# Kernel optimization log

Hardware: AMD Instinct MI355X
Metric: run time of the kernel (lower is better)

Reference implementation:

```python
import jax, jax.numpy as jnp
import numpy as np
from jax.scipy.special import gammaln

S, N, T = 8, 32, 262144
EPS = 1e-16  # emission clamp, as in torch .clamp(min=1e-16)


def setup_inputs() -> dict:
    key = jax.random.key(0)
    k1, k2, k3, k4 = jax.random.split(key, 4)
    spikes = jax.random.randint(k1, (T, N), 0, 2).astype(jnp.int32)  # binary counts
    convolved_spikes = 0.5 * jax.random.normal(k2, (T, N), dtype=jnp.float32)
    weight = 0.1 * jax.random.normal(k3, (S, N, N), dtype=jnp.float32)
    bias = 0.1 * jax.random.normal(k4, (N,), dtype=jnp.float32)
    eye = jnp.eye(S, dtype=jnp.float32)
    transition_matrix = eye * 0.98 + (0.02 / (S - 1)) * (1.0 - eye)
    return {"spikes": spikes, "convolved_spikes": convolved_spikes,
            "weight": weight, "bias": bias, "transition_matrix": transition_matrix}


def reference(spikes, convolved_spikes, weight, bias, transition_matrix):
    n_states = weight.shape[0]
    init_p = jnp.ones(n_states, dtype=convolved_spikes.dtype) / n_states
    A = transition_matrix  # (S, S)

    # firing_rates: sigmoid(bias + conv @ W[s].T) -> (S, T, N)
    rates = jax.nn.sigmoid(bias[None, None, :] +
                           jnp.einsum('tn,smn->stm', convolved_spikes, weight))
    x = spikes.astype(rates.dtype)
    # Poisson log-likelihood summed over neurons, then (S,T) -> (T,S)
    log_emission = (x[None] * jnp.log(rates) - rates - gammaln(x + 1.0)[None]).sum(-1).T

    emission = jnp.clip(jnp.exp(log_emission), EPS)  # (T, S)

    # forward pass (scaling)
    a0 = init_p * emission[0]
    c0 = a0.sum()
    a0 = a0 / c0

    def fstep(a_prev, em_t):
        a = em_t * (A.T @ a_prev)
        c = a.sum()
        an = a / c
        return an, (an, c)

    _, (alpha_rest, c_rest) = jax.lax.scan(fstep, a0, emission[1:])
    alpha = jnp.concatenate([a0[None], alpha_rest])  # (T, S)
    c = jnp.concatenate([c0[None], c_rest])          # (T,)

    # backward pass
    def bstep(b_next, ec):
        em_t1, c_t1 = ec
        b = A @ (b_next * em_t1) / c_t1
        return b, b

    b_last = jnp.ones(n_states, dtype=emission.dtype)
    _, beta_head = jax.lax.scan(bstep, b_last, (emission[1:], c[1:]), reverse=True)
    beta = jnp.concatenate([beta_head, b_last[None]])  # (T, S)

    gamma = alpha * beta  # (T, S)
    xi = (alpha[:-1, :, None] * emission[1:, None, :] *
          A[None, :, :] * beta[1:, None, :]) / c[1:, None, None]  # (T-1, S, S)
    return gamma, xi
```

## Files before the change

kernel.cpp:

```cpp
#include <hip/hip_runtime.h>
#include <math.h>


constexpr int TT  = 262144;
constexpr int LL  = 64;
constexpr int CK  = TT / LL;
constexpr int CPG = 16;
constexpr int NG  = CK / CPG;
constexpr int NSG = 16;
constexpr int EP  = 516;

typedef __attribute__((ext_vector_type(8))) short bf16x8;
typedef __attribute__((ext_vector_type(4))) float f32x4;

__device__ __forceinline__ float rcp_nr(float x) {
  float r = __builtin_amdgcn_rcpf(x);
  return r * (2.0f - x * r);
}
__device__ __forceinline__ unsigned short f2bf(float f) {
  unsigned u = __float_as_uint(f);
  u += 0x7FFFu + ((u >> 16) & 1u);
  return (unsigned short)(u >> 16);
}
__device__ __forceinline__ float bf2f(unsigned short h) {
  return __uint_as_float(((unsigned)h) << 16);
}

#define SWZ8(x, k) __int_as_float(__builtin_amdgcn_ds_swizzle(__float_as_int(x), (((k) << 5) | 0x18)))
#define SWZX(x, d) __int_as_float(__builtin_amdgcn_ds_swizzle(__float_as_int(x), (((d) << 10) | 0x1F)))
#define BPERM(a, x) __int_as_float(__builtin_amdgcn_ds_bpermute((a), __float_as_int(x)))

#define TREE8(dst, v) { float s01=v[0]+v[1], s23=v[2]+v[3], s45=v[4]+v[5], s67=v[6]+v[7]; dst = (s01+s23)+(s45+s67); }

__global__ __launch_bounds__(256) void k_emission(
    const int* __restrict__ spikes, const float* __restrict__ conv,
    const float* __restrict__ W, const float* __restrict__ bias,
    float* __restrict__ em, float* __restrict__ iemax) {
  __shared__ short sWbf[256 * 40];
  __shared__ unsigned sMask[64];
  const int tid = threadIdx.x;
  const int lane = tid & 63;
  const int wv = tid >> 6;
  const int T0 = blockIdx.x * 64;
  const int q = lane & 15;
  const int rg = lane >> 4;

#pragma unroll
  for (int it = 0; it < 8; ++it) {
    int idx4 = tid + it * 256;
    float4 w4 = ((const float4*)W)[idx4];
    int sm = idx4 >> 3, n0 = (idx4 & 7) << 2;
    ushort4 h;
    h.x = f2bf(w4.x); h.y = f2bf(w4.y); h.z = f2bf(w4.z); h.w = f2bf(w4.w);
    *(ushort4*)&sWbf[sm * 40 + n0] = h;
  }
#pragma unroll
  for (int it = 0; it < 8; ++it) {
    int idx = it * 256 + tid;
    int t = idx >> 5;
    int v = spikes[(size_t)(T0 + t) * 32 + (idx & 31)];
    unsigned long long b = __ballot(v != 0);
    if ((lane & 31) == 0) sMask[t] = (unsigned)(b >> (lane & 32));
  }
  __syncthreads();

  const int tg0 = T0 + wv * 16;
  const float* cp = conv + (size_t)(tg0 + q) * 32 + rg * 8;
  float4 ca = *(const float4*)cp;
  float4 cb = *(const float4*)(cp + 4);
  bf16x8 ch, cl;
  {
    float cv[8] = {ca.x, ca.y, ca.z, ca.w, cb.x, cb.y, cb.z, cb.w};
#pragma unroll
    for (int e2 = 0; e2 < 8; ++e2) {
      unsigned short hb = f2bf(cv[e2]);
      ch[e2] = (short)hb;
      cl[e2] = (short)f2bf(cv[e2] - bf2f(hb));
    }
  }
  const float4 bl4 = ((const float4*)bias)[rg];
  const float4 bh4 = ((const float4*)bias)[rg + 4];
  const float bjlo[4] = {bl4.x, bl4.y, bl4.z, bl4.w};
  const float bjhi[4] = {bh4.x, bh4.y, bh4.z, bh4.w};
  const unsigned mk = sMask[wv * 16 + q];
  constexpr float L2E = 1.4426950408889634f;
  const f32x4 zacc = {0.f, 0.f, 0.f, 0.f};

  bf16x8 wfr[16];
#pragma unroll
  for (int t16 = 0; t16 < 16; ++t16)
    wfr[t16] = *(bf16x8*)&sWbf[(t16 * 16 + q) * 40 + rg * 8];

  float e[8];
  float mx = 0.f;
#pragma unroll
  for (int sp = 0; sp < 8; ++sp) {
    f32x4 a0 = __builtin_amdgcn_mfma_f32_16x16x32_bf16(wfr[2 * sp], cl, zacc, 0, 0, 0);
    a0 = __builtin_amdgcn_mfma_f32_16x16x32_bf16(wfr[2 * sp], ch, a0, 0, 0, 0);
    f32x4 a1 = __builtin_amdgcn_mfma_f32_16x16x32_bf16(wfr[2 * sp + 1], cl, zacc, 0, 0, 0);
    a1 = __builtin_amdgcn_mfma_f32_16x16x32_bf16(wfr[2 * sp + 1], ch, a1, 0, 0, 0);
    float sumr = 0.f, pr = 1.f;
#pragma unroll
    for (int r = 0; r < 4; ++r) {
      float z0 = a0[r] + bjlo[r];
      float u0 = __builtin_amdgcn_exp2f(z0 * -L2E);
      float p0 = 1.f + u0;
      sumr += __builtin_amdgcn_rcpf(p0);
      pr *= ((mk >> (rg * 4 + r)) & 1u) ? p0 : 1.f;
      float z1 = a1[r] + bjhi[r];
      float u1 = __builtin_amdgcn_exp2f(z1 * -L2E);
      float p1 = 1.f + u1;
      sumr += __builtin_amdgcn_rcpf(p1);
      pr *= ((mk >> (16 + rg * 4 + r)) & 1u) ? p1 : 1.f;
    }
    float g = fmaf(-L2E, sumr, -__builtin_amdgcn_logf(pr));
    g += SWZX(g, 16);
    g += __shfl_xor(g, 32);
    float ev = fmaxf(__builtin_amdgcn_exp2f(g), 1e-16f);
    e[sp] = ev;
    mx = fmaxf(mx, ev);
  }
  if (lane < 16) {
    float4 o0 = {e[0], e[1], e[2], e[3]};
    float4 o1 = {e[4], e[5], e[6], e[7]};
    *(float4*)&em[(size_t)(tg0 + q) * 8] = o0;
    *(float4*)&em[(size_t)(tg0 + q) * 8 + 4] = o1;
    iemax[tg0 + q] = rcp_nr(mx);
  }
}

__global__ __launch_bounds__(128) void k_fwd_chunks(
    const float* __restrict__ em, const float* __restrict__ iemax,
    const float* __restrict__ A, float* __restrict__ Pf,
    float* __restrict__ Gf) {
  __shared__ float sE[16 * EP];
  __shared__ float sM[16 * 64];
  const int tid = threadIdx.x;
  const int cl = tid >> 3, jc = tid & 7;
  const int c = blockIdx.x * 16 + cl;
  const float b_ = A[1];
  const float aa = A[0] - b_;

  for (int idx = tid; idx < 8192; idx += 128) {
    int gi = blockIdx.x * 8192 + idx;
    sE[(idx >> 9) * EP + (idx & 511)] = em[gi] * iemax[gi >> 3];
  }
  __syncthreads();

  float p[8];
#pragma unroll
  for (int k = 0; k < 8; ++k) p[k] = (k == jc) ? 1.f : 0.f;
  const float* eb = &sE[cl * EP];
#pragma unroll 8
  for (int t = 0; t < 64; ++t) {
    float4 e0 = *(const float4*)&eb[t * 8];
    float4 e1 = *(const float4*)&eb[t * 8 + 4];
    float e[8] = {e0.x, e0.y, e0.z, e0.w, e1.x, e1.y, e1.z, e1.w};
    if (c == 0 && t == 0) {
#pragma unroll
      for (int r = 0; r < 8; ++r) p[r] = e[r] * p[r];
    } else {
      float sg; TREE8(sg, p);
      float bs = b_ * sg;
#pragma unroll
      for (int r = 0; r < 8; ++r) p[r] = e[r] * fmaf(aa, p[r], bs);
    }
    if ((t & 7) == 7) {
      float m = p[0];
#pragma unroll
      for (int k = 1; k < 8; ++k) m = fmaxf(m, p[k]);
      m = fmaxf(m, SWZX(m, 1)); m = fmaxf(m, SWZX(m, 2)); m = fmaxf(m, SWZX(m, 4));
      float rm = __builtin_amdgcn_rcpf(m);
#pragma unroll
      for (int k = 0; k < 8; ++k) p[k] *= rm;
    }
  }
#pragma unroll
  for (int r = 0; r < 8; ++r) {
    sM[cl * 64 + r * 8 + jc] = p[r];
    Pf[(size_t)c * 64 + r * 8 + jc] = p[r];
  }
  __syncthreads();

  if (tid < 64) {
    const int L = tid;
    int ad[8];
#pragma unroll
    for (int k = 0; k < 8; ++k) ad[k] = (((k << 3) | (L & 7))) << 2;
    float S = sM[L];
    for (int m = 1; m < 16; ++m) {
      float4 r0 = *(const float4*)&sM[m * 64 + (L >> 3) * 8];
      float4 r1 = *(const float4*)&sM[m * 64 + (L >> 3) * 8 + 4];
      float acc;
      acc =      r0.x * BPERM(ad[0], S);
      acc = fmaf(r0.y,  BPERM(ad[1], S), acc);
      acc = fmaf(r0.z,  BPERM(ad[2], S), acc);
      acc = fmaf(r0.w,  BPERM(ad[3], S), acc);
      acc = fmaf(r1.x,  BPERM(ad[4], S), acc);
      acc = fmaf(r1.y,  BPERM(ad[5], S), acc);
      acc = fmaf(r1.z,  BPERM(ad[6], S), acc);
      acc = fmaf(r1.w,  BPERM(ad[7], S), acc);
      S = acc;
      if ((m & 3) == 3) {
        float mx = S;
        mx = fmaxf(mx, SWZX(mx, 1));  mx = fmaxf(mx, SWZX(mx, 2));
        mx = fmaxf(mx, SWZX(mx, 4));  mx = fmaxf(mx, SWZX(mx, 8));
        mx = fmaxf(mx, SWZX(mx, 16)); mx = fmaxf(mx, __shfl_xor(mx, 32));
        S *= __builtin_amdgcn_rcpf(mx);
      }
    }
    Gf[(size_t)blockIdx.x * 64 + L] = S;
  }
}

__global__ __launch_bounds__(1024) void k_fwd_mid(
    const float* __restrict__ Gf, float* __restrict__ vg) {
  __shared__ float sG[NG * 64];
  __shared__ float sgS[NSG * 64];
  __shared__ float sgE[NSG * 8];
  const int tid = threadIdx.x, wv = tid >> 6, L = tid & 63;
  for (int idx = tid; idx < NG * 64; idx += 1024) sG[idx] = Gf[idx];
  __syncthreads();

  int ad[8];
#pragma unroll
  for (int k = 0; k < 8; ++k) ad[k] = (((k << 3) | (L & 7))) << 2;
  const int ad2 = ((L & 7) * 9) << 2;

  {
    float S = sG[wv * 1024 + L];
    for (int m = 1; m < 16; ++m) {
      const float* mb = &sG[(wv * 16 + m) * 64 + (L >> 3) * 8];
      float4 r0 = *(const float4*)mb;
      float4 r1 = *(const float4*)(mb + 4);
      float acc;
      acc =      r0.x * BPERM(ad[0], S);
      acc = fmaf(r0.y,  BPERM(ad[1], S), acc);
      acc = fmaf(r0.z,  BPERM(ad[2], S), acc);
      acc = fmaf(r0.w,  BPERM(ad[3], S), acc);
      acc = fmaf(r1.x,  BPERM(ad[4], S), acc);
      acc = fmaf(r1.y,  BPERM(ad[5], S), acc);
      acc = fmaf(r1.z,  BPERM(ad[6], S), acc);
      acc = fmaf(r1.w,  BPERM(ad[7], S), acc);
      S = acc;
      if ((m & 3) == 3) {
        float mx = S;
        mx = fmaxf(mx, SWZX(mx, 1));  mx = fmaxf(mx, SWZX(mx, 2));
        mx = fmaxf(mx, SWZX(mx, 4));  mx = fmaxf(mx, SWZX(mx, 8));
        mx = fmaxf(mx, SWZX(mx, 16)); mx = fmaxf(mx, __shfl_xor(mx, 32));
        S *= __builtin_amdgcn_rcpf(mx);
      }
    }
    sgS[wv * 64 + L] = S;
  }
  __syncthreads();

  if (wv == 0) {
    float vj = 0.125f;
    for (int sg = 0; sg < 16; ++sg) {
      if (L < 8) sgE[sg * 8 + L] = vj;
      float t = sgS[sg * 64 + L] * vj;
      t += SWZX(t, 1); t += SWZX(t, 2); t += SWZX(t, 4);
      float t2 = t + SWZX(t, 8); t2 += SWZX(t2, 16); t2 += __shfl_xor(t2, 32);
      vj = BPERM(ad2, t) * rcp_nr(t2);
    }
  }
  __syncthreads();

  {
    float vj = sgE[wv * 8 + (L & 7)];
    for (int gl = 0; gl < 16; ++gl) {
      int g = wv * 16 + gl;
      if (L < 8) vg[g * 8 + L] = vj;
      float t = sG[g * 64 + L] * vj;
      t += SWZX(t, 1); t += SWZX(t, 2); t += SWZX(t, 4);
      float t2 = t + SWZX(t, 8); t2 += SWZX(t2, 16); t2 += __shfl_xor(t2, 32);
      vj = BPERM(ad2, t) * rcp_nr(t2);
    }
  }
}

__global__ __launch_bounds__(128) void k_frbc(
    const float* __restrict__ em, const float* __restrict__ A,
    const float* __restrict__ vg, float* __restrict__ bf,
    float* __restrict__ alpha, float* __restrict__ cvec,
    float* __restrict__ PfRb, float* __restrict__ Gb) {
  __shared__ float sE[16 * EP];
  __shared__ float sRC[16 * 66];
  __shared__ float sBf[16 * 8];
  __shared__ float sM[16 * 64];
  const int tid = threadIdx.x;
  const int cl = tid >> 3, jl = tid & 7;
  const int c = blockIdx.x * 16 + cl;
  const float b_ = A[1];
  const float aa = A[0] - b_;

  for (int idx = tid; idx < 8192; idx += 128)
    sE[(idx >> 9) * EP + (idx & 511)] = em[(size_t)blockIdx.x * 8192 + idx];

  if (tid < 64) {
    const int L = tid;
    const int ad2 = ((L & 7) * 9) << 2;
    float f[16];
#pragma unroll
    for (int m = 0; m < 16; ++m) f[m] = PfRb[(size_t)(blockIdx.x * 16 + m) * 64 + L];
    float vj = vg[blockIdx.x * 8 + (L & 7)];
#pragma unroll
    for (int m = 0; m < 16; ++m) {
      if (L < 8) {
        sBf[m * 8 + L] = vj;
        bf[(size_t)(blockIdx.x * 16 + m) * 8 + L] = vj;
      }
      float t = f[m] * vj;
      t += SWZX(t, 1); t += SWZX(t, 2); t += SWZX(t, 4);
      float t2 = t + SWZX(t, 8); t2 += SWZX(t2, 16); t2 += __shfl_xor(t2, 32);
      vj = BPERM(ad2, t) * rcp_nr(t2);
    }
  }
  __syncthreads();

  {
    float u[8];
#pragma unroll
    for (int k = 0; k < 8; ++k) u[k] = sBf[cl * 8 + k];
    float rs = 1.f;
    const float* eb = &sE[cl * EP];
#pragma unroll 4
    for (int t = 0; t < 64; ++t) {
      float4 e0 = *(const float4*)&eb[t * 8];
      float4 e1 = *(const float4*)&eb[t * 8 + 4];
      float e[8] = {e0.x, e0.y, e0.z, e0.w, e1.x, e1.y, e1.z, e1.w};
      float un[8];
      if (c == 0 && t == 0) {
#pragma unroll
        for (int r = 0; r < 8; ++r) un[r] = 0.125f * e[r];
      } else {
        float sg; TREE8(sg, u);
        float bs = b_ * sg;
#pragma unroll
        for (int r = 0; r < 8; ++r) un[r] = (e[r] * rs) * fmaf(aa, u[r], bs);
      }
      float s; TREE8(s, un);
      float rsn = rcp_nr(s);
      float myu = un[0];
#pragma unroll
      for (int k = 1; k < 8; ++k) myu = (jl == k) ? un[k] : myu;
      int tg = c * 64 + t;
      alpha[(size_t)tg * 8 + jl] = myu * rsn;
      if (jl == 0) { cvec[tg] = s; sRC[cl * 66 + t] = rsn; }
#pragma unroll
      for (int k = 0; k < 8; ++k) u[k] = un[k];
      rs = rsn;
    }
  }
  __syncthreads();

  {
    float rv[8];
#pragma unroll
    for (int k = 0; k < 8; ++k) rv[k] = (k == jl) ? 1.f : 0.f;
    const float* eb = &sE[cl * EP];
    const float* rb = &sRC[cl * 66];
#pragma unroll 4
    for (int t = 0; t < 64; ++t) {
      float rc = rb[t];
      float4 d0 = *(const float4*)&eb[t * 8];
      float4 d1 = *(const float4*)&eb[t * 8 + 4];
      float d[8] = {d0.x * rc, d0.y * rc, d0.z * rc, d0.w * rc,
                    d1.x * rc, d1.y * rc, d1.z * rc, d1.w * rc};
      float sg; TREE8(sg, rv);
      float bs = b_ * sg;
#pragma unroll
      for (int j = 0; j < 8; ++j) rv[j] = fmaf(aa, rv[j], bs) * d[j];
    }
    float4 o0 = {rv[0], rv[1], rv[2], rv[3]};
    float4 o1 = {rv[4], rv[5], rv[6], rv[7]};
    *(float4*)&sM[cl * 64 + jl * 8] = o0;
    *(float4*)&sM[cl * 64 + jl * 8 + 4] = o1;
    *(float4*)&PfRb[(size_t)c * 64 + jl * 8] = o0;
    *(float4*)&PfRb[(size_t)c * 64 + jl * 8 + 4] = o1;
  }
  __syncthreads();

  if (tid < 64) {
    const int L = tid;
    float S = sM[L];
    for (int m = 1; m < 16; ++m) {
      const float* mb = &sM[m * 64 + (L & 7)];
      float acc;
      acc =      SWZ8(S, 0) * mb[0];
      acc = fmaf(SWZ8(S, 1), mb[8],  acc);
      acc = fmaf(SWZ8(S, 2), mb[16], acc);
      acc = fmaf(SWZ8(S, 3), mb[24], acc);
      acc = fmaf(SWZ8(S, 4), mb[32], acc);
      acc = fmaf(SWZ8(S, 5), mb[40], acc);
      acc = fmaf(SWZ8(S, 6), mb[48], acc);
      acc = fmaf(SWZ8(S, 7), mb[56], acc);
      S = acc;
    }
    Gb[(size_t)blockIdx.x * 64 + L] = S;
  }
}

__global__ __launch_bounds__(1024) void k_bwd_mid(
    const float* __restrict__ Gb, float* __restrict__ wg) {
  __shared__ float sG[NG * 64];
  __shared__ float sgS[NSG * 64];
  __shared__ float sgE[NSG * 8];
  const int tid = threadIdx.x, wv = tid >> 6, L = tid & 63;
  for (int idx = tid; idx < NG * 64; idx += 1024) sG[idx] = Gb[idx];
  __syncthreads();

  const int ad2 = ((L & 7) * 9) << 2;
  {
    float S = sG[wv * 1024 + L];
    for (int m = 1; m < 16; ++m) {
      const float* mb = &sG[(wv * 16 + m) * 64 + (L & 7)];
      float acc;
      acc =      SWZ8(S, 0) * mb[0];
      acc = fmaf(SWZ8(S, 1), mb[8],  acc);
      acc = fmaf(SWZ8(S, 2), mb[16], acc);
      acc = fmaf(SWZ8(S, 3), mb[24], acc);
      acc = fmaf(SWZ8(S, 4), mb[32], acc);
      acc = fmaf(SWZ8(S, 5), mb[40], acc);
      acc = fmaf(SWZ8(S, 6), mb[48], acc);
      acc = fmaf(SWZ8(S, 7), mb[56], acc);
      S = acc;
    }
    sgS[wv * 64 + L] = S;
  }
  __syncthreads();

  if (wv == 0) {
    float wj = 1.f;
    for (int sg = 15; sg >= 0; --sg) {
      if (L < 8) sgE[sg * 8 + L] = wj;
      float t = sgS[sg * 64 + L] * wj;
      t += SWZX(t, 1); t += SWZX(t, 2); t += SWZX(t, 4);
      wj = BPERM(ad2, t);
    }
  }
  __syncthreads();

  {
    float wj = sgE[wv * 8 + (L & 7)];
    for (int gl = 15; gl >= 0; --gl) {
      int g = wv * 16 + gl;
      if (L < 8) wg[g * 8 + L] = wj;
      float t = sG[g * 64 + L] * wj;
      t += SWZX(t, 1); t += SWZX(t, 2); t += SWZX(t, 4);
      wj = BPERM(ad2, t);
    }
  }
}

__global__ __launch_bounds__(1024) void k_bwd_replay(
    const float* __restrict__ em, const float* __restrict__ cvec,
    const float* __restrict__ A, const float* __restrict__ bf,
    const float* __restrict__ wg, const float* __restrict__ Rb,
    float* __restrict__ gamma, float* __restrict__ xi) {
  __shared__ float sQ[16 * 512];
  __shared__ float sAl[16 * 512];
  __shared__ float sGb[16 * 8];
  const int tid = threadIdx.x, wv = tid >> 6, L = tid & 63;
  const int i = L >> 3, j = L & 7;
  const int c = blockIdx.x * 16 + wv;
  const float Aij = A[i * 8 + j];

  for (int idx = tid; idx < 8192; idx += 1024) {
    int gi = blockIdx.x * 8192 + idx;
    sQ[idx] = em[gi] * rcp_nr(cvec[gi >> 3]);
    int cl2 = idx >> 9, rr = (idx >> 3) & 63, s = idx & 7;
    float av;
    if (rr == 0) av = bf[(blockIdx.x * 16 + cl2) * 8 + s];
    else av = gamma[((size_t)(blockIdx.x * 16 + cl2) * 64 + rr - 1) * 8 + s];
    sAl[idx] = av;
  }
  if (wv == 0) {
    const int ad2 = ((L & 7) * 9) << 2;
    float f[16];
#pragma unroll
    for (int m = 0; m < 16; ++m) f[m] = Rb[(size_t)(blockIdx.x * 16 + m) * 64 + L];
    float vj = wg[blockIdx.x * 8 + (L & 7)];
#pragma unroll
    for (int m = 15; m >= 0; --m) {
      if (L < 8) sGb[m * 8 + L] = vj;
      float t = f[m] * vj;
      t += SWZX(t, 1); t += SWZX(t, 2); t += SWZX(t, 4);
      vj = BPERM(ad2, t);
    }
  }
  __syncthreads();

  float b = sGb[wv * 8 + j];
  {
    int te = c * 64 + 63;
    if (L < 8) {
      float al = gamma[(size_t)te * 8 + L];
      gamma[(size_t)te * 8 + L] = al * b;
    }
  }
#pragma unroll 4
  for (int t = 63; t >= 0; --t) {
    int tg = c * 64 + t;
    float q = sQ[wv * 512 + t * 8 + j] * b;
    float apv = sAl[wv * 512 + t * 8 + i];
    if (tg > 0) xi[(size_t)(tg - 1) * 64 + L] = apv * Aij * q;
    float p = Aij * q;
    p += SWZX(p, 1); p += SWZX(p, 2); p += SWZX(p, 4);
    if (t > 0 && j == 0) gamma[(size_t)(tg - 1) * 8 + i] = apv * p;
    b = __shfl(p, (L & 7) * 8);
  }
}

extern "C" void kernel_launch(void* const* d_in, const int* in_sizes, int n_in,
                              void* d_out, int out_size, void* d_ws, size_t ws_size,
                              hipStream_t stream) {
  const int*   spikes = (const int*)  d_in[0];
  const float* conv   = (const float*)d_in[1];
  const float* W      = (const float*)d_in[2];
  const float* bias   = (const float*)d_in[3];
  const float* A      = (const float*)d_in[4];

  float* out   = (float*)d_out;
  float* gamma = out;
  float* xi    = out + (size_t)TT * 8;

  float* ws    = (float*)d_ws;
  float* em    = ws;
  float* iemax = em + (size_t)TT * 8;
  float* cvec  = iemax + TT;
  float* Pf    = cvec + TT;
  float* Rb    = Pf;
  float* Gf    = Pf + (size_t)CK * 64;
  float* Gb    = Gf;
  float* vg    = Gf + NG * 64;
  float* wg    = vg + NG * 8;
  float* bf    = wg + NG * 8;
  (void)in_sizes; (void)n_in; (void)out_size; (void)ws_size;

  k_emission  <<<TT / 64, 256, 0, stream>>>(spikes, conv, W, bias, em, iemax);
  k_fwd_chunks<<<NG, 128, 0, stream>>>(em, iemax, A, Pf, Gf);
  k_fwd_mid   <<<1, 1024, 0, stream>>>(Gf, vg);
  k_frbc      <<<NG, 128, 0, stream>>>(em, A, vg, bf, gamma, cvec, Pf, Gb);
  k_bwd_mid   <<<1, 1024, 0, stream>>>(Gb, wg);
  k_bwd_replay<<<NG, 1024, 0, stream>>>(em, cvec, A, bf, wg, Rb, gamma, xi);
}
```

Before: 126.5 us.

## Fuse all HMM stages into one cooperative persistent kernel with grid syncs

Replaces the six-kernel pipeline with a single cooperative kernel of NG=256 blocks of 1024 threads. Emissions, scaled alpha, beta and the per-chunk state all stay in shared memory, so the global round-trips of em, iemax, cvec, alpha and the Pf/Rb buffers go away. The single-block mid-level scans become grid.sync-separated phases, and each block recomputes its own group prefix instead of reading a precomputed vector. In exchange it pays for several grid-wide barriers, leaves most threads idle during the serial chunk and scan phases, and puts heavy register and LDS pressure on 1024-thread blocks.

```diff
diff --git a/kernel.cpp b/kernel.cpp
--- a/kernel.cpp
+++ b/kernel.cpp
@@ -1,5 +1,8 @@
 #include <hip/hip_runtime.h>
+#include <hip/hip_cooperative_groups.h>
 #include <math.h>
+
+namespace cg = cooperative_groups;
 
 
 constexpr int TT  = 262144;
@@ -29,25 +32,38 @@
 #define SWZ8(x, k) __int_as_float(__builtin_amdgcn_ds_swizzle(__float_as_int(x), (((k) << 5) | 0x18)))
 #define SWZX(x, d) __int_as_float(__builtin_amdgcn_ds_swizzle(__float_as_int(x), (((d) << 10) | 0x1F)))
 #define BPERM(a, x) __int_as_float(__builtin_amdgcn_ds_bpermute((a), __float_as_int(x)))
-
 #define TREE8(dst, v) { float s01=v[0]+v[1], s23=v[2]+v[3], s45=v[4]+v[5], s67=v[6]+v[7]; dst = (s01+s23)+(s45+s67); }
 
-__global__ __launch_bounds__(256) void k_emission(
+__global__ __launch_bounds__(1024, 4) void k_all(
     const int* __restrict__ spikes, const float* __restrict__ conv,
     const float* __restrict__ W, const float* __restrict__ bias,
-    float* __restrict__ em, float* __restrict__ iemax) {
+    const float* __restrict__ A,
+    float* __restrict__ gamma, float* __restrict__ xi,
+    float* __restrict__ Gf, float* __restrict__ sgSf, float* __restrict__ sgEf,
+    float* __restrict__ Gb, float* __restrict__ sgSb, float* __restrict__ sgEb) {
+  cg::grid_group gg = cg::this_grid();
+
+  __shared__ float sEm[16 * EP];
+  __shared__ float sAl[16 * EP];
+  __shared__ float sIex[16 * 66];
+  __shared__ float sRc[16 * 66];
+  __shared__ unsigned sMask[1024];
   __shared__ short sWbf[256 * 40];
-  __shared__ unsigned sMask[64];
-  const int tid = threadIdx.x;
-  const int lane = tid & 63;
-  const int wv = tid >> 6;
-  const int T0 = blockIdx.x * 64;
-  const int q = lane & 15;
-  const int rg = lane >> 4;
-
-#pragma unroll
-  for (int it = 0; it < 8; ++it) {
-    int idx4 = tid + it * 256;
+  __shared__ float sM[16 * 64];
+  __shared__ float sBf[16 * 8];
+  __shared__ float sGbv[16 * 8];
+  __shared__ float sVg[8];
+  __shared__ float sWgv[8];
+
+  const int tid = threadIdx.x, lane = tid & 63, wv = tid >> 6;
+  const int bid = blockIdx.x;
+  const float b_ = A[1];
+  const float aa = A[0] - b_;
+  constexpr float L2E = 1.4426950408889634f;
+
+#pragma unroll
+  for (int it = 0; it < 2; ++it) {
+    int idx4 = tid + it * 1024;
     float4 w4 = ((const float4*)W)[idx4];
     int sm = idx4 >> 3, n0 = (idx4 & 7) << 2;
     ushort4 h;
@@ -55,139 +71,123 @@
     *(ushort4*)&sWbf[sm * 40 + n0] = h;
   }
 #pragma unroll
-  for (int it = 0; it < 8; ++it) {
-    int idx = it * 256 + tid;
+  for (int it = 0; it < 32; ++it) {
+    int idx = it * 1024 + tid;
     int t = idx >> 5;
-    int v = spikes[(size_t)(T0 + t) * 32 + (idx & 31)];
-    unsigned long long b = __ballot(v != 0);
-    if ((lane & 31) == 0) sMask[t] = (unsigned)(b >> (lane & 32));
-  }
-  __syncthreads();
-
-  const int tg0 = T0 + wv * 16;
-  const float* cp = conv + (size_t)(tg0 + q) * 32 + rg * 8;
-  float4 ca = *(const float4*)cp;
-  float4 cb = *(const float4*)(cp + 4);
-  bf16x8 ch, cl;
+    int v = spikes[(size_t)(bid * 1024 + t) * 32 + (idx & 31)];
+    unsigned long long bl = __ballot(v != 0);
+    if ((lane & 31) == 0) sMask[t] = (unsigned)(bl >> (lane & 32));
+  }
+  __syncthreads();
+
   {
-    float cv[8] = {ca.x, ca.y, ca.z, ca.w, cb.x, cb.y, cb.z, cb.w};
-#pragma unroll
-    for (int e2 = 0; e2 < 8; ++e2) {
-      unsigned short hb = f2bf(cv[e2]);
-      ch[e2] = (short)hb;
-      cl[e2] = (short)f2bf(cv[e2] - bf2f(hb));
-    }
-  }
-  const float4 bl4 = ((const float4*)bias)[rg];
-  const float4 bh4 = ((const float4*)bias)[rg + 4];
-  const float bjlo[4] = {bl4.x, bl4.y, bl4.z, bl4.w};
-  const float bjhi[4] = {bh4.x, bh4.y, bh4.z, bh4.w};
-  const unsigned mk = sMask[wv * 16 + q];
-  constexpr float L2E = 1.4426950408889634f;
-  const f32x4 zacc = {0.f, 0.f, 0.f, 0.f};
-
-  bf16x8 wfr[16];
-#pragma unroll
-  for (int t16 = 0; t16 < 16; ++t16)
-    wfr[t16] = *(bf16x8*)&sWbf[(t16 * 16 + q) * 40 + rg * 8];
-
-  float e[8];
-  float mx = 0.f;
-#pragma unroll
-  for (int sp = 0; sp < 8; ++sp) {
-    f32x4 a0 = __builtin_amdgcn_mfma_f32_16x16x32_bf16(wfr[2 * sp], cl, zacc, 0, 0, 0);
-    a0 = __builtin_amdgcn_mfma_f32_16x16x32_bf16(wfr[2 * sp], ch, a0, 0, 0, 0);
-    f32x4 a1 = __builtin_amdgcn_mfma_f32_16x16x32_bf16(wfr[2 * sp + 1], cl, zacc, 0, 0, 0);
-    a1 = __builtin_amdgcn_mfma_f32_16x16x32_bf16(wfr[2 * sp + 1], ch, a1, 0, 0, 0);
-    float sumr = 0.f, pr = 1.f;
-#pragma unroll
-    for (int r = 0; r < 4; ++r) {
-      float z0 = a0[r] + bjlo[r];
-      float u0 = __builtin_amdgcn_exp2f(z0 * -L2E);
-      float p0 = 1.f + u0;
-      sumr += __builtin_amdgcn_rcpf(p0);
-      pr *= ((mk >> (rg * 4 + r)) & 1u) ? p0 : 1.f;
-      float z1 = a1[r] + bjhi[r];
-      float u1 = __builtin_amdgcn_exp2f(z1 * -L2E);
-      float p1 = 1.f + u1;
-      sumr += __builtin_amdgcn_rcpf(p1);
-      pr *= ((mk >> (16 + rg * 4 + r)) & 1u) ? p1 : 1.f;
-    }
-    float g = fmaf(-L2E, sumr, -__builtin_amdgcn_logf(pr));
-    g += SWZX(g, 16);
-    g += __shfl_xor(g, 32);
-    float ev = fmaxf(__builtin_amdgcn_exp2f(g), 1e-16f);
-    e[sp] = ev;
-    mx = fmaxf(mx, ev);
-  }
-  if (lane < 16) {
-    float4 o0 = {e[0], e[1], e[2], e[3]};
-    float4 o1 = {e[4], e[5], e[6], e[7]};
-    *(float4*)&em[(size_t)(tg0 + q) * 8] = o0;
-    *(float4*)&em[(size_t)(tg0 + q) * 8 + 4] = o1;
-    iemax[tg0 + q] = rcp_nr(mx);
-  }
-}
-
-__global__ __launch_bounds__(128) void k_fwd_chunks(
-    const float* __restrict__ em, const float* __restrict__ iemax,
-    const float* __restrict__ A, float* __restrict__ Pf,
-    float* __restrict__ Gf) {
-  __shared__ float sE[16 * EP];
-  __shared__ float sM[16 * 64];
-  const int tid = threadIdx.x;
-  const int cl = tid >> 3, jc = tid & 7;
-  const int c = blockIdx.x * 16 + cl;
-  const float b_ = A[1];
-  const float aa = A[0] - b_;
-
-  for (int idx = tid; idx < 8192; idx += 128) {
-    int gi = blockIdx.x * 8192 + idx;
-    sE[(idx >> 9) * EP + (idx & 511)] = em[gi] * iemax[gi >> 3];
-  }
-  __syncthreads();
-
-  float p[8];
-#pragma unroll
-  for (int k = 0; k < 8; ++k) p[k] = (k == jc) ? 1.f : 0.f;
-  const float* eb = &sE[cl * EP];
-#pragma unroll 8
-  for (int t = 0; t < 64; ++t) {
-    float4 e0 = *(const float4*)&eb[t * 8];
-    float4 e1 = *(const float4*)&eb[t * 8 + 4];
-    float e[8] = {e0.x, e0.y, e0.z, e0.w, e1.x, e1.y, e1.z, e1.w};
-    if (c == 0 && t == 0) {
-#pragma unroll
-      for (int r = 0; r < 8; ++r) p[r] = e[r] * p[r];
-    } else {
-      float sg; TREE8(sg, p);
-      float bs = b_ * sg;
-#pragma unroll
-      for (int r = 0; r < 8; ++r) p[r] = e[r] * fmaf(aa, p[r], bs);
-    }
-    if ((t & 7) == 7) {
-      float m = p[0];
-#pragma unroll
-      for (int k = 1; k < 8; ++k) m = fmaxf(m, p[k]);
-      m = fmaxf(m, SWZX(m, 1)); m = fmaxf(m, SWZX(m, 2)); m = fmaxf(m, SWZX(m, 4));
-      float rm = __builtin_amdgcn_rcpf(m);
-#pragma unroll
-      for (int k = 0; k < 8; ++k) p[k] *= rm;
-    }
-  }
-#pragma unroll
-  for (int r = 0; r < 8; ++r) {
-    sM[cl * 64 + r * 8 + jc] = p[r];
-    Pf[(size_t)c * 64 + r * 8 + jc] = p[r];
-  }
-  __syncthreads();
-
+    const int q = lane & 15, rg = lane >> 4;
+    const float4 bl4 = ((const float4*)bias)[rg];
+    const float4 bh4 = ((const float4*)bias)[rg + 4];
+    const float bjlo[4] = {bl4.x, bl4.y, bl4.z, bl4.w};
+    const float bjhi[4] = {bh4.x, bh4.y, bh4.z, bh4.w};
+    const f32x4 zacc = {0.f, 0.f, 0.f, 0.f};
+    for (int itt = 0; itt < 4; ++itt) {
+      const int tl = itt * 16 + q;
+      const int Tg = bid * 1024 + wv * 64 + tl;
+      const float* cp = conv + (size_t)Tg * 32 + rg * 8;
+      float4 ca = *(const float4*)cp;
+      float4 cb = *(const float4*)(cp + 4);
+      bf16x8 ch, cfl;
+      {
+        float cv[8] = {ca.x, ca.y, ca.z, ca.w, cb.x, cb.y, cb.z, cb.w};
+#pragma unroll
+        for (int e2 = 0; e2 < 8; ++e2) {
+          unsigned short hb = f2bf(cv[e2]);
+          ch[e2] = (short)hb;
+          cfl[e2] = (short)f2bf(cv[e2] - bf2f(hb));
+        }
+      }
+      const unsigned mk = sMask[wv * 64 + tl];
+      float e[8];
+      float mx = 0.f;
+#pragma unroll
+      for (int sp = 0; sp < 8; ++sp) {
+        bf16x8 wf0 = *(bf16x8*)&sWbf[((2 * sp) * 16 + q) * 40 + rg * 8];
+        f32x4 a0 = __builtin_amdgcn_mfma_f32_16x16x32_bf16(wf0, cfl, zacc, 0, 0, 0);
+        a0 = __builtin_amdgcn_mfma_f32_16x16x32_bf16(wf0, ch, a0, 0, 0, 0);
+        bf16x8 wf1 = *(bf16x8*)&sWbf[((2 * sp + 1) * 16 + q) * 40 + rg * 8];
+        f32x4 a1 = __builtin_amdgcn_mfma_f32_16x16x32_bf16(wf1, cfl, zacc, 0, 0, 0);
+        a1 = __builtin_amdgcn_mfma_f32_16x16x32_bf16(wf1, ch, a1, 0, 0, 0);
+        float sumr = 0.f, pr = 1.f;
+#pragma unroll
+        for (int r = 0; r < 4; ++r) {
+          float z0 = a0[r] + bjlo[r];
+          float u0 = __builtin_amdgcn_exp2f(z0 * -L2E);
+          float p0 = 1.f + u0;
+          sumr += __builtin_amdgcn_rcpf(p0);
+          pr *= ((mk >> (rg * 4 + r)) & 1u) ? p0 : 1.f;
+          float z1 = a1[r] + bjhi[r];
+          float u1 = __builtin_amdgcn_exp2f(z1 * -L2E);
+          float p1 = 1.f + u1;
+          sumr += __builtin_amdgcn_rcpf(p1);
+          pr *= ((mk >> (16 + rg * 4 + r)) & 1u) ? p1 : 1.f;
+        }
+        float g = fmaf(-L2E, sumr, -__builtin_amdgcn_logf(pr));
+        g += SWZX(g, 16);
+        g += __shfl_xor(g, 32);
+        float ev = fmaxf(__builtin_amdgcn_exp2f(g), 1e-16f);
+        e[sp] = ev;
+        mx = fmaxf(mx, ev);
+      }
+      if (lane < 16) {
+        float4 o0 = {e[0], e[1], e[2], e[3]};
+        float4 o1 = {e[4], e[5], e[6], e[7]};
+        *(float4*)&sEm[wv * EP + tl * 8] = o0;
+        *(float4*)&sEm[wv * EP + tl * 8 + 4] = o1;
+        sIex[wv * 66 + tl] = rcp_nr(mx);
+      }
+    }
+  }
+  __syncthreads();
+
+  if (tid < 128) {
+    const int cl = tid >> 3, jc = tid & 7;
+    float p[8];
+#pragma unroll
+    for (int k = 0; k < 8; ++k) p[k] = (k == jc) ? 1.f : 0.f;
+    const float* eb = &sEm[cl * EP];
+    for (int t = 0; t < 64; ++t) {
+      float iex = sIex[cl * 66 + t];
+      float4 e0 = *(const float4*)&eb[t * 8];
+      float4 e1 = *(const float4*)&eb[t * 8 + 4];
+      float e[8] = {e0.x * iex, e0.y * iex, e0.z * iex, e0.w * iex,
+                    e1.x * iex, e1.y * iex, e1.z * iex, e1.w * iex};
+      if (bid == 0 && cl == 0 && t == 0) {
+#pragma unroll
+        for (int r = 0; r < 8; ++r) p[r] = e[r] * p[r];
+      } else {
+        float sg; TREE8(sg, p);
+        float bs = b_ * sg;
+#pragma unroll
+        for (int r = 0; r < 8; ++r) p[r] = e[r] * fmaf(aa, p[r], bs);
+      }
+      if ((t & 7) == 7) {
+        float m = p[0];
+#pragma unroll
+        for (int k = 1; k < 8; ++k) m = fmaxf(m, p[k]);
+        m = fmaxf(m, SWZX(m, 1)); m = fmaxf(m, SWZX(m, 2)); m = fmaxf(m, SWZX(m, 4));
+        float rm = __builtin_amdgcn_rcpf(m);
+#pragma unroll
+        for (int k = 0; k < 8; ++k) p[k] *= rm;
+      }
+    }
+#pragma unroll
+    for (int r = 0; r < 8; ++r) sM[cl * 64 + r * 8 + jc] = p[r];
+  }
+  __syncthreads();
   if (tid < 64) {
     const int L = tid;
     int ad[8];
 #pragma unroll
     for (int k = 0; k < 8; ++k) ad[k] = (((k << 3) | (L & 7))) << 2;
     float S = sM[L];
+#pragma unroll
     for (int m = 1; m < 16; ++m) {
       float4 r0 = *(const float4*)&sM[m * 64 + (L >> 3) * 8];
       float4 r1 = *(const float4*)&sM[m * 64 + (L >> 3) * 8 + 4];
@@ -209,28 +209,19 @@
         S *= __builtin_amdgcn_rcpf(mx);
       }
     }
-    Gf[(size_t)blockIdx.x * 64 + L] = S;
-  }
-}
-
-__global__ __launch_bounds__(1024) void k_fwd_mid(
-    const float* __restrict__ Gf, float* __restrict__ vg) {
-  __shared__ float sG[NG * 64];
-  __shared__ float sgS[NSG * 64];
-  __shared__ float sgE[NSG * 8];
-  const int tid = threadIdx.x, wv = tid >> 6, L = tid & 63;
-  for (int idx = tid; idx < NG * 64; idx += 1024) sG[idx] = Gf[idx];
-  __syncthreads();
-
-  int ad[8];
-#pragma unroll
-  for (int k = 0; k < 8; ++k) ad[k] = (((k << 3) | (L & 7))) << 2;
-  const int ad2 = ((L & 7) * 9) << 2;
-
-  {
-    float S = sG[wv * 1024 + L];
+    Gf[(size_t)bid * 64 + L] = S;
+  }
+  gg.sync();
+
+  if (bid < NSG && tid < 64) {
+    const int L = tid;
+    int ad[8];
+#pragma unroll
+    for (int k = 0; k < 8; ++k) ad[k] = (((k << 3) | (L & 7))) << 2;
+    float S = Gf[(size_t)(bid * 16) * 64 + L];
+#pragma unroll
     for (int m = 1; m < 16; ++m) {
-      const float* mb = &sG[(wv * 16 + m) * 64 + (L >> 3) * 8];
+      const float* mb = &Gf[(size_t)(bid * 16 + m) * 64 + (L >> 3) * 8];
       float4 r0 = *(const float4*)mb;
       float4 r1 = *(const float4*)(mb + 4);
       float acc;
@@ -251,66 +242,55 @@
         S *= __builtin_amdgcn_rcpf(mx);
       }
     }
-    sgS[wv * 64 + L] = S;
-  }
-  __syncthreads();
-
-  if (wv == 0) {
+    sgSf[bid * 64 + L] = S;
+  }
+  gg.sync();
+  if (bid == 0 && tid < 64) {
+    const int L = tid;
+    const int ad2 = ((L & 7) * 9) << 2;
     float vj = 0.125f;
     for (int sg = 0; sg < 16; ++sg) {
-      if (L < 8) sgE[sg * 8 + L] = vj;
-      float t = sgS[sg * 64 + L] * vj;
+      if (L < 8) sgEf[sg * 8 + L] = vj;
+      float t = sgSf[sg * 64 + L] * vj;
       t += SWZX(t, 1); t += SWZX(t, 2); t += SWZX(t, 4);
       float t2 = t + SWZX(t, 8); t2 += SWZX(t2, 16); t2 += __shfl_xor(t2, 32);
       vj = BPERM(ad2, t) * rcp_nr(t2);
     }
   }
-  __syncthreads();
-
+  gg.sync();
   {
-    float vj = sgE[wv * 8 + (L & 7)];
-    for (int gl = 0; gl < 16; ++gl) {
-      int g = wv * 16 + gl;
-      if (L < 8) vg[g * 8 + L] = vj;
-      float t = sG[g * 64 + L] * vj;
-      t += SWZX(t, 1); t += SWZX(t, 2); t += SWZX(t, 4);
-      float t2 = t + SWZX(t, 8); t2 += SWZX(t2, 16); t2 += __shfl_xor(t2, 32);
-      vj = BPERM(ad2, t) * rcp_nr(t2);
-    }
-  }
-}
-
-__global__ __launch_bounds__(128) void k_frbc(
-    const float* __restrict__ em, const float* __restrict__ A,
-    const float* __restrict__ vg, float* __restrict__ bf,
-    float* __restrict__ alpha, float* __restrict__ cvec,
-    float* __restrict__ PfRb, float* __restrict__ Gb) {
-  __shared__ float sE[16 * EP];
-  __shared__ float sRC[16 * 66];
-  __shared__ float sBf[16 * 8];
-  __shared__ float sM[16 * 64];
-  const int tid = threadIdx.x;
-  const int cl = tid >> 3, jl = tid & 7;
-  const int c = blockIdx.x * 16 + cl;
-  const float b_ = A[1];
-  const float aa = A[0] - b_;
-
-  for (int idx = tid; idx < 8192; idx += 128)
-    sE[(idx >> 9) * EP + (idx & 511)] = em[(size_t)blockIdx.x * 8192 + idx];
+    const int sg = bid >> 4, kk = bid & 15;
+    if (tid < 64) {
+      const int L = tid;
+      const int ad2 = ((L & 7) * 9) << 2;
+      float f[15];
+#pragma unroll
+      for (int m = 0; m < 15; ++m) f[m] = Gf[(size_t)(sg * 16 + m) * 64 + L];
+      float vj = sgEf[sg * 8 + (L & 7)];
+#pragma unroll
+      for (int m = 0; m < 15; ++m) {
+        if (m < kk) {
+          float t = f[m] * vj;
+          t += SWZX(t, 1); t += SWZX(t, 2); t += SWZX(t, 4);
+          float t2 = t + SWZX(t, 8); t2 += SWZX(t2, 16); t2 += __shfl_xor(t2, 32);
+          vj = BPERM(ad2, t) * rcp_nr(t2);
+        }
+      }
+      if (L < 8) sVg[L] = vj;
+    }
+  }
+  __syncthreads();
 
   if (tid < 64) {
     const int L = tid;
     const int ad2 = ((L & 7) * 9) << 2;
     float f[16];
 #pragma unroll
-    for (int m = 0; m < 16; ++m) f[m] = PfRb[(size_t)(blockIdx.x * 16 + m) * 64 + L];
-    float vj = vg[blockIdx.x * 8 + (L & 7)];
+    for (int m = 0; m < 16; ++m) f[m] = sM[m * 64 + L];
+    float vj = sVg[L & 7];
 #pragma unroll
     for (int m = 0; m < 16; ++m) {
-      if (L < 8) {
-        sBf[m * 8 + L] = vj;
-        bf[(size_t)(blockIdx.x * 16 + m) * 8 + L] = vj;
-      }
+      if (L < 8) sBf[m * 8 + L] = vj;
       float t = f[m] * vj;
       t += SWZX(t, 1); t += SWZX(t, 2); t += SWZX(t, 4);
       float t2 = t + SWZX(t, 8); t2 += SWZX(t2, 16); t2 += __shfl_xor(t2, 32);
@@ -318,20 +298,19 @@
     }
   }
   __syncthreads();
-
   {
     float u[8];
 #pragma unroll
-    for (int k = 0; k < 8; ++k) u[k] = sBf[cl * 8 + k];
+    for (int k = 0; k < 8; ++k) u[k] = sBf[wv * 8 + k];
     float rs = 1.f;
-    const float* eb = &sE[cl * EP];
+    const float* eb = &sEm[wv * EP];
 #pragma unroll 4
     for (int t = 0; t < 64; ++t) {
       float4 e0 = *(const float4*)&eb[t * 8];
       float4 e1 = *(const float4*)&eb[t * 8 + 4];
       float e[8] = {e0.x, e0.y, e0.z, e0.w, e1.x, e1.y, e1.z, e1.w};
       float un[8];
-      if (c == 0 && t == 0) {
+      if (bid == 0 && wv == 0 && t == 0) {
 #pragma unroll
         for (int r = 0; r < 8; ++r) un[r] = 0.125f * e[r];
       } else {
@@ -344,10 +323,9 @@
       float rsn = rcp_nr(s);
       float myu = un[0];
 #pragma unroll
-      for (int k = 1; k < 8; ++k) myu = (jl == k) ? un[k] : myu;
-      int tg = c * 64 + t;
-      alpha[(size_t)tg * 8 + jl] = myu * rsn;
-      if (jl == 0) { cvec[tg] = s; sRC[cl * 66 + t] = rsn; }
+      for (int k = 1; k < 8; ++k) myu = (lane == k) ? un[k] : myu;
+      if (lane < 8) sAl[wv * EP + t * 8 + lane] = myu * rsn;
+      if (lane == 0) sRc[wv * 66 + t] = rsn;
 #pragma unroll
       for (int k = 0; k < 8; ++k) u[k] = un[k];
       rs = rsn;
@@ -356,14 +334,14 @@
   __syncthreads();
 
   {
+    const int il = lane & 7;
     float rv[8];
 #pragma unroll
-    for (int k = 0; k < 8; ++k) rv[k] = (k == jl) ? 1.f : 0.f;
-    const float* eb = &sE[cl * EP];
-    const float* rb = &sRC[cl * 66];
+    for (int k = 0; k < 8; ++k) rv[k] = (k == il) ? 1.f : 0.f;
+    const float* eb = &sEm[wv * EP];
 #pragma unroll 4
     for (int t = 0; t < 64; ++t) {
-      float rc = rb[t];
+      float rc = sRc[wv * 66 + t];
       float4 d0 = *(const float4*)&eb[t * 8];
       float4 d1 = *(const float4*)&eb[t * 8 + 4];
       float d[8] = {d0.x * rc, d0.y * rc, d0.z * rc, d0.w * rc,
@@ -373,18 +351,18 @@
 #pragma unroll
       for (int j = 0; j < 8; ++j) rv[j] = fmaf(aa, rv[j], bs) * d[j];
     }
-    float4 o0 = {rv[0], rv[1], rv[2], rv[3]};
-    float4 o1 = {rv[4], rv[5], rv[6], rv[7]};
-    *(float4*)&sM[cl * 64 + jl * 8] = o0;
-    *(float4*)&sM[cl * 64 + jl * 8 + 4] = o1;
-    *(float4*)&PfRb[(size_t)c * 64 + jl * 8] = o0;
-    *(float4*)&PfRb[(size_t)c * 64 + jl * 8 + 4] = o1;
-  }
-  __syncthreads();
-
+    if (lane < 8) {
+      float4 o0 = {rv[0], rv[1], rv[2], rv[3]};
+      float4 o1 = {rv[4], rv[5], rv[6], rv[7]};
+      *(float4*)&sM[wv * 64 + lane * 8] = o0;
+      *(float4*)&sM[wv * 64 + lane * 8 + 4] = o1;
+    }
+  }
+  __syncthreads();
   if (tid < 64) {
     const int L = tid;
     float S = sM[L];
+#pragma unroll
     for (int m = 1; m < 16; ++m) {
       const float* mb = &sM[m * 64 + (L & 7)];
       float acc;
@@ -398,24 +376,16 @@
       acc = fmaf(SWZ8(S, 7), mb[56], acc);
       S = acc;
     }
-    Gb[(size_t)blockIdx.x * 64 + L] = S;
-  }
-}
-
-__global__ __launch_bounds__(1024) void k_bwd_mid(
-    const float* __restrict__ Gb, float* __restrict__ wg) {
-  __shared__ float sG[NG * 64];
-  __shared__ float sgS[NSG * 64];
-  __shared__ float sgE[NSG * 8];
-  const int tid = threadIdx.x, wv = tid >> 6, L = tid & 63;
-  for (int idx = tid; idx < NG * 64; idx += 1024) sG[idx] = Gb[idx];
-  __syncthreads();
-
-  const int ad2 = ((L & 7) * 9) << 2;
-  {
-    float S = sG[wv * 1024 + L];
+    Gb[(size_t)bid * 64 + L] = S;
+  }
+  gg.sync();
+
+  if (bid < NSG && tid < 64) {
+    const int L = tid;
+    float S = Gb[(size_t)(bid * 16) * 64 + L];
+#pragma unroll
     for (int m = 1; m < 16; ++m) {
-      const float* mb = &sG[(wv * 16 + m) * 64 + (L & 7)];
+      const float* mb = &Gb[(size_t)(bid * 16 + m) * 64 + (L & 7)];
       float acc;
       acc =      SWZ8(S, 0) * mb[0];
       acc = fmaf(SWZ8(S, 1), mb[8],  acc);
@@ -427,89 +397,79 @@
       acc = fmaf(SWZ8(S, 7), mb[56], acc);
       S = acc;
     }
-    sgS[wv * 64 + L] = S;
-  }
-  __syncthreads();
-
-  if (wv == 0) {
+    sgSb[bid * 64 + L] = S;
+  }
+  gg.sync();
+  if (bid == 0 && tid < 64) {
+    const int L = tid;
+    const int ad2 = ((L & 7) * 9) << 2;
     float wj = 1.f;
     for (int sg = 15; sg >= 0; --sg) {
-      if (L < 8) sgE[sg * 8 + L] = wj;
-      float t = sgS[sg * 64 + L] * wj;
+      if (L < 8) sgEb[sg * 8 + L] = wj;
+      float t = sgSb[sg * 64 + L] * wj;
       t += SWZX(t, 1); t += SWZX(t, 2); t += SWZX(t, 4);
       wj = BPERM(ad2, t);
     }
   }
-  __syncthreads();
-
+  gg.sync();
   {
-    float wj = sgE[wv * 8 + (L & 7)];
-    for (int gl = 15; gl >= 0; --gl) {
-      int g = wv * 16 + gl;
-      if (L < 8) wg[g * 8 + L] = wj;
-      float t = sG[g * 64 + L] * wj;
-      t += SWZX(t, 1); t += SWZX(t, 2); t += SWZX(t, 4);
-      wj = BPERM(ad2, t);
-    }
-  }
-}
-
-__global__ __launch_bounds__(1024) void k_bwd_replay(
-    const float* __restrict__ em, const float* __restrict__ cvec,
-    const float* __restrict__ A, const float* __restrict__ bf,
-    const float* __restrict__ wg, const float* __restrict__ Rb,
-    float* __restrict__ gamma, float* __restrict__ xi) {
-  __shared__ float sQ[16 * 512];
-  __shared__ float sAl[16 * 512];
-  __shared__ float sGb[16 * 8];
-  const int tid = threadIdx.x, wv = tid >> 6, L = tid & 63;
-  const int i = L >> 3, j = L & 7;
-  const int c = blockIdx.x * 16 + wv;
-  const float Aij = A[i * 8 + j];
-
-  for (int idx = tid; idx < 8192; idx += 1024) {
-    int gi = blockIdx.x * 8192 + idx;
-    sQ[idx] = em[gi] * rcp_nr(cvec[gi >> 3]);
-    int cl2 = idx >> 9, rr = (idx >> 3) & 63, s = idx & 7;
-    float av;
-    if (rr == 0) av = bf[(blockIdx.x * 16 + cl2) * 8 + s];
-    else av = gamma[((size_t)(blockIdx.x * 16 + cl2) * 64 + rr - 1) * 8 + s];
-    sAl[idx] = av;
-  }
-  if (wv == 0) {
+    const int sg = bid >> 4, kk = bid & 15;
+    if (tid < 64) {
+      const int L = tid;
+      const int ad2 = ((L & 7) * 9) << 2;
+      float f[15];
+#pragma unroll
+      for (int gl = 1; gl < 16; ++gl) f[gl - 1] = Gb[(size_t)(sg * 16 + gl) * 64 + L];
+      float wj = sgEb[sg * 8 + (L & 7)];
+#pragma unroll
+      for (int gl = 15; gl >= 1; --gl) {
+        if (gl > kk) {
+          float t = f[gl - 1] * wj;
+          t += SWZX(t, 1); t += SWZX(t, 2); t += SWZX(t, 4);
+          wj = BPERM(ad2, t);
+        }
+      }
+      if (L < 8) sWgv[L] = wj;
+    }
+  }
+  __syncthreads();
+
+  if (tid < 64) {
+    const int L = tid;
     const int ad2 = ((L & 7) * 9) << 2;
     float f[16];
 #pragma unroll
-    for (int m = 0; m < 16; ++m) f[m] = Rb[(size_t)(blockIdx.x * 16 + m) * 64 + L];
-    float vj = wg[blockIdx.x * 8 + (L & 7)];
+    for (int m = 0; m < 16; ++m) f[m] = sM[m * 64 + L];
+    float vj = sWgv[L & 7];
 #pragma unroll
     for (int m = 15; m >= 0; --m) {
-      if (L < 8) sGb[m * 8 + L] = vj;
+      if (L < 8) sGbv[m * 8 + L] = vj;
       float t = f[m] * vj;
       t += SWZX(t, 1); t += SWZX(t, 2); t += SWZX(t, 4);
       vj = BPERM(ad2, t);
     }
   }
   __syncthreads();
-
-  float b = sGb[wv * 8 + j];
   {
-    int te = c * 64 + 63;
-    if (L < 8) {
-      float al = gamma[(size_t)te * 8 + L];
-      gamma[(size_t)te * 8 + L] = al * b;
-    }
-  }
+    const int i = lane >> 3, j = lane & 7;
+    const int c = bid * 16 + wv;
+    const float Aij = A[i * 8 + j];
+    float b = sGbv[wv * 8 + j];
+    if (lane < 8) {
+      float al = sAl[wv * EP + 63 * 8 + lane];
+      gamma[(size_t)(c * 64 + 63) * 8 + lane] = al * b;
+    }
 #pragma unroll 4
-  for (int t = 63; t >= 0; --t) {
-    int tg = c * 64 + t;
-    float q = sQ[wv * 512 + t * 8 + j] * b;
-    float apv = sAl[wv * 512 + t * 8 + i];
-    if (tg > 0) xi[(size_t)(tg - 1) * 64 + L] = apv * Aij * q;
-    float p = Aij * q;
-    p += SWZX(p, 1); p += SWZX(p, 2); p += SWZX(p, 4);
-    if (t > 0 && j == 0) gamma[(size_t)(tg - 1) * 8 + i] = apv * p;
-    b = __shfl(p, (L & 7) * 8);
+    for (int t = 63; t >= 0; --t) {
+      int tg = c * 64 + t;
+      float qv = sEm[wv * EP + t * 8 + j] * sRc[wv * 66 + t] * b;
+      float apv = (t == 0) ? sBf[wv * 8 + i] : sAl[wv * EP + (t - 1) * 8 + i];
+      if (tg > 0) xi[(size_t)(tg - 1) * 64 + lane] = apv * Aij * qv;
+      float p = Aij * qv;
+      p += SWZX(p, 1); p += SWZX(p, 2); p += SWZX(p, 4);
+      if (t > 0 && j == 0) gamma[(size_t)(tg - 1) * 8 + i] = apv * p;
+      b = __shfl(p, (lane & 7) * 8);
+    }
   }
 }
 
@@ -527,22 +487,17 @@
   float* xi    = out + (size_t)TT * 8;
 
   float* ws    = (float*)d_ws;
-  float* em    = ws;
-  float* iemax = em + (size_t)TT * 8;
-  float* cvec  = iemax + TT;
-  float* Pf    = cvec + TT;
-  float* Rb    = Pf;
-  float* Gf    = Pf + (size_t)CK * 64;
-  float* Gb    = Gf;
-  float* vg    = Gf + NG * 64;
-  float* wg    = vg + NG * 8;
-  float* bf    = wg + NG * 8;
+  float* Gf    = ws;
+  float* sgSf  = Gf + (size_t)NG * 64;
+  float* sgEf  = sgSf + NSG * 64;
+  float* Gb    = sgEf + NSG * 8;
+  float* sgSb  = Gb + (size_t)NG * 64;
+  float* sgEb  = sgSb + NSG * 64;
   (void)in_sizes; (void)n_in; (void)out_size; (void)ws_size;
 
-  k_emission  <<<TT / 64, 256, 0, stream>>>(spikes, conv, W, bias, em, iemax);
-  k_fwd_chunks<<<NG, 128, 0, stream>>>(em, iemax, A, Pf, Gf);
-  k_fwd_mid   <<<1, 1024, 0, stream>>>(Gf, vg);
-  k_frbc      <<<NG, 128, 0, stream>>>(em, A, vg, bf, gamma, cvec, Pf, Gb);
-  k_bwd_mid   <<<1, 1024, 0, stream>>>(Gb, wg);
-  k_bwd_replay<<<NG, 1024, 0, stream>>>(em, cvec, A, bf, wg, Rb, gamma, xi);
+  void* args[] = {(void*)&spikes, (void*)&conv, (void*)&W, (void*)&bias,
+                  (void*)&A, (void*)&gamma, (void*)&xi,
+                  (void*)&Gf, (void*)&sgSf, (void*)&sgEf,
+                  (void*)&Gb, (void*)&sgSb, (void*)&sgEb};
+  hipLaunchCooperativeKernel((void*)k_all, dim3(NG), dim3(1024), args, 0, stream);
 }
```

Result: slower. 287.3 us (+127.1%).

## Use 32x32x16 MFMA in emission kernel with 128 timesteps per block

Applied to the files above, without the earlier changes.

The emission kernel switches from 16x16x32 bf16 MFMAs to 32x32x16 MFMAs, so each wave handles 32 timesteps instead of 16 and each block covers 128 timesteps, halving the grid. Each lane now holds 16 output rows, which removes one cross-lane swizzle reduction and amortizes the per-block weight conversion to bf16 in shared memory over twice as many timesteps. Weight fragments are read from LDS inside the state loop instead of being preloaded into registers. The trade-offs are higher register pressure from 16-wide accumulators and fewer blocks, which may reduce the latency hiding available.

```diff
diff --git a/kernel.cpp b/kernel.cpp
--- a/kernel.cpp
+++ b/kernel.cpp
@@ -10,8 +10,9 @@
 constexpr int NSG = 16;
 constexpr int EP  = 516;
 
-typedef __attribute__((ext_vector_type(8))) short bf16x8;
-typedef __attribute__((ext_vector_type(4))) float f32x4;
+typedef __attribute__((ext_vector_type(8)))  short bf16x8;
+typedef __attribute__((ext_vector_type(4)))  float f32x4;
+typedef __attribute__((ext_vector_type(16))) float f32x16;
 
 __device__ __forceinline__ float rcp_nr(float x) {
   float r = __builtin_amdgcn_rcpf(x);
@@ -37,13 +38,13 @@
     const float* __restrict__ W, const float* __restrict__ bias,
     float* __restrict__ em, float* __restrict__ iemax) {
   __shared__ short sWbf[256 * 40];
-  __shared__ unsigned sMask[64];
+  __shared__ unsigned sMask[128];
   const int tid = threadIdx.x;
   const int lane = tid & 63;
   const int wv = tid >> 6;
-  const int T0 = blockIdx.x * 64;
-  const int q = lane & 15;
-  const int rg = lane >> 4;
+  const int T0 = blockIdx.x * 128;
+  const int tcol = lane & 31;
+  const int hi = lane >> 5;
 
 #pragma unroll
   for (int it = 0; it < 8; ++it) {
@@ -55,7 +56,7 @@
     *(ushort4*)&sWbf[sm * 40 + n0] = h;
   }
 #pragma unroll
-  for (int it = 0; it < 8; ++it) {
+  for (int it = 0; it < 16; ++it) {
     int idx = it * 256 + tid;
     int t = idx >> 5;
     int v = spikes[(size_t)(T0 + t) * 32 + (idx & 31)];
@@ -64,68 +65,71 @@
   }
   __syncthreads();
 
-  const int tg0 = T0 + wv * 16;
-  const float* cp = conv + (size_t)(tg0 + q) * 32 + rg * 8;
-  float4 ca = *(const float4*)cp;
-  float4 cb = *(const float4*)(cp + 4);
-  bf16x8 ch, cl;
-  {
-    float cv[8] = {ca.x, ca.y, ca.z, ca.w, cb.x, cb.y, cb.z, cb.w};
+  const int tg = T0 + wv * 32 + tcol;
+  const float* cp = conv + (size_t)tg * 32 + hi * 8;
+  float4 c0a = *(const float4*)cp;
+  float4 c0b = *(const float4*)(cp + 4);
+  float4 c1a = *(const float4*)(cp + 16);
+  float4 c1b = *(const float4*)(cp + 20);
+  bf16x8 ch0, cl0, ch1, cl1;
+  {
+    float cv0[8] = {c0a.x, c0a.y, c0a.z, c0a.w, c0b.x, c0b.y, c0b.z, c0b.w};
+    float cv1[8] = {c1a.x, c1a.y, c1a.z, c1a.w, c1b.x, c1b.y, c1b.z, c1b.w};
 #pragma unroll
     for (int e2 = 0; e2 < 8; ++e2) {
-      unsigned short hb = f2bf(cv[e2]);
-      ch[e2] = (short)hb;
-      cl[e2] = (short)f2bf(cv[e2] - bf2f(hb));
-    }
-  }
-  const float4 bl4 = ((const float4*)bias)[rg];
-  const float4 bh4 = ((const float4*)bias)[rg + 4];
-  const float bjlo[4] = {bl4.x, bl4.y, bl4.z, bl4.w};
-  const float bjhi[4] = {bh4.x, bh4.y, bh4.z, bh4.w};
-  const unsigned mk = sMask[wv * 16 + q];
+      unsigned short h0 = f2bf(cv0[e2]);
+      ch0[e2] = (short)h0;
+      cl0[e2] = (short)f2bf(cv0[e2] - bf2f(h0));
+      unsigned short h1 = f2bf(cv1[e2]);
+      ch1[e2] = (short)h1;
+      cl1[e2] = (short)f2bf(cv1[e2] - bf2f(h1));
+    }
+  }
+  float bj[16];
+#pragma unroll
+  for (int g = 0; g < 4; ++g) {
+    float4 b4 = *(const float4*)&bias[hi * 4 + g * 8];
+    bj[g * 4 + 0] = b4.x; bj[g * 4 + 1] = b4.y;
+    bj[g * 4 + 2] = b4.z; bj[g * 4 + 3] = b4.w;
+  }
+  const unsigned mk = sMask[wv * 32 + tcol];
   constexpr float L2E = 1.4426950408889634f;
-  const f32x4 zacc = {0.f, 0.f, 0.f, 0.f};
-
-  bf16x8 wfr[16];
-#pragma unroll
-  for (int t16 = 0; t16 < 16; ++t16)
-    wfr[t16] = *(bf16x8*)&sWbf[(t16 * 16 + q) * 40 + rg * 8];
+  f32x16 zacc;
+#pragma unroll
+  for (int r = 0; r < 16; ++r) zacc[r] = 0.f;
 
   float e[8];
   float mx = 0.f;
 #pragma unroll
-  for (int sp = 0; sp < 8; ++sp) {
-    f32x4 a0 = __builtin_amdgcn_mfma_f32_16x16x32_bf16(wfr[2 * sp], cl, zacc, 0, 0, 0);
-    a0 = __builtin_amdgcn_mfma_f32_16x16x32_bf16(wfr[2 * sp], ch, a0, 0, 0, 0);
-    f32x4 a1 = __builtin_amdgcn_mfma_f32_16x16x32_bf16(wfr[2 * sp + 1], cl, zacc, 0, 0, 0);
-    a1 = __builtin_amdgcn_mfma_f32_16x16x32_bf16(wfr[2 * sp + 1], ch, a1, 0, 0, 0);
+  for (int s = 0; s < 8; ++s) {
+    bf16x8 A0 = *(bf16x8*)&sWbf[(s * 32 + tcol) * 40 + hi * 8];
+    bf16x8 A1 = *(bf16x8*)&sWbf[(s * 32 + tcol) * 40 + 16 + hi * 8];
+    f32x16 acc = __builtin_amdgcn_mfma_f32_32x32x16_bf16(A0, cl0, zacc, 0, 0, 0);
+    acc = __builtin_amdgcn_mfma_f32_32x32x16_bf16(A1, cl1, acc, 0, 0, 0);
+    acc = __builtin_amdgcn_mfma_f32_32x32x16_bf16(A0, ch0, acc, 0, 0, 0);
+    acc = __builtin_amdgcn_mfma_f32_32x32x16_bf16(A1, ch1, acc, 0, 0, 0);
     float sumr = 0.f, pr = 1.f;
 #pragma unroll
-    for (int r = 0; r < 4; ++r) {
-      float z0 = a0[r] + bjlo[r];
-      float u0 = __builtin_amdgcn_exp2f(z0 * -L2E);
-      float p0 = 1.f + u0;
-      sumr += __builtin_amdgcn_rcpf(p0);
-      pr *= ((mk >> (rg * 4 + r)) & 1u) ? p0 : 1.f;
-      float z1 = a1[r] + bjhi[r];
-      float u1 = __builtin_amdgcn_exp2f(z1 * -L2E);
-      float p1 = 1.f + u1;
-      sumr += __builtin_amdgcn_rcpf(p1);
-      pr *= ((mk >> (16 + rg * 4 + r)) & 1u) ? p1 : 1.f;
+    for (int r = 0; r < 16; ++r) {
+      float z = acc[r] + bj[r];
+      float u = __builtin_amdgcn_exp2f(z * -L2E);
+      float p = 1.f + u;
+      sumr += __builtin_amdgcn_rcpf(p);
+      int m = (r & 3) + 8 * (r >> 2) + 4 * hi;
+      pr *= ((mk >> m) & 1u) ? p : 1.f;
     }
     float g = fmaf(-L2E, sumr, -__builtin_amdgcn_logf(pr));
-    g += SWZX(g, 16);
     g += __shfl_xor(g, 32);
     float ev = fmaxf(__builtin_amdgcn_exp2f(g), 1e-16f);
-    e[sp] = ev;
+    e[s] = ev;
     mx = fmaxf(mx, ev);
   }
-  if (lane < 16) {
+  if (lane < 32) {
     float4 o0 = {e[0], e[1], e[2], e[3]};
     float4 o1 = {e[4], e[5], e[6], e[7]};
-    *(float4*)&em[(size_t)(tg0 + q) * 8] = o0;
-    *(float4*)&em[(size_t)(tg0 + q) * 8 + 4] = o1;
-    iemax[tg0 + q] = rcp_nr(mx);
+    *(float4*)&em[(size_t)tg * 8] = o0;
+    *(float4*)&em[(size_t)tg * 8 + 4] = o1;
+    iemax[tg] = rcp_nr(mx);
   }
 }
 
@@ -539,7 +543,7 @@
   float* bf    = wg + NG * 8;
   (void)in_sizes; (void)n_in; (void)out_size; (void)ws_size;
 
-  k_emission  <<<TT / 64, 256, 0, stream>>>(spikes, conv, W, bias, em, iemax);
+  k_emission  <<<TT / 128, 256, 0, stream>>>(spikes, conv, W, bias, em, iemax);
   k_fwd_chunks<<<NG, 128, 0, stream>>>(em, iemax, A, Pf, Gf);
   k_fwd_mid   <<<1, 1024, 0, stream>>>(Gf, vg);
   k_frbc      <<<NG, 128, 0, stream>>>(em, A, vg, bf, gamma, cvec, Pf, Gb);
```

Result: faster. 124.0 us (-2.0%).
